# Optimization experiments

Hardware: AMD Instinct MI355X
Metric: run time of the kernel (lower is better)

## Reference

```python
import jax, jax.numpy as jnp
import numpy as np

FEA, DK, H = 768, 64, 12
B, L = 4, 1024
MASK_VAL = -2**15 + 1  # matches torch masked_fill constant


def setup_inputs() -> dict:
    key = jax.random.key(0)
    ks = jax.random.split(key, 16)
    d = {
        'qx': jax.random.normal(ks[0], (B, L, FEA), jnp.float32),
        'kx': jax.random.normal(ks[1], (B, L, FEA), jnp.float32),
        'vx': jax.random.normal(ks[2], (B, L, FEA), jnp.float32),
        'preScores': jax.random.normal(ks[3], (B, H, L, L), jnp.float32),
        'maskPAD': jax.random.randint(ks[4], (B, L, L), 0, 2, jnp.int32),
    }
    s = 1.0 / np.sqrt(FEA)
    d['WQ_w'] = jax.random.normal(ks[5], (H * DK, FEA), jnp.float32) * s
    d['WQ_b'] = jnp.zeros((H * DK,), jnp.float32)
    d['WK_w'] = jax.random.normal(ks[6], (H * DK, FEA), jnp.float32) * s
    d['WK_b'] = jnp.zeros((H * DK,), jnp.float32)
    d['WV_w'] = jax.random.normal(ks[7], (H * DK, FEA), jnp.float32) * s
    d['WV_b'] = jnp.zeros((H * DK,), jnp.float32)
    d['WO_w'] = jax.random.normal(ks[8], (FEA, H * DK), jnp.float32) * s
    d['WO_b'] = jnp.zeros((FEA,), jnp.float32)
    return d


def reference(qx, kx, vx, preScores, maskPAD,
              WQ_w, WQ_b, WK_w, WK_b, WV_w, WV_b, WO_w, WO_b):
    b, l, c = qx.shape
    # projections -> (B, H, L, dk)
    q = (qx @ WQ_w.T + WQ_b).reshape(b, l, H, DK).transpose(0, 2, 1, 3)
    k = (kx @ WK_w.T + WK_b).reshape(b, l, H, DK).transpose(0, 2, 1, 3)
    v = (vx @ WV_w.T + WV_b).reshape(b, l, H, DK).transpose(0, 2, 1, 3)
    scores = jnp.einsum('bhqd,bhkd->bhqk', q, k) / np.sqrt(DK)
    scores = scores + preScores  # RealFormer residual scores
    scores = jnp.where((maskPAD == 0)[:, None, :, :], jnp.float32(MASK_VAL), scores)
    alpha = jax.nn.softmax(scores, axis=3)  # dropout p=0 (eval/deterministic)
    z = jnp.einsum('bhqk,bhkd->bhqd', alpha, v)
    z = z.transpose(0, 2, 1, 3).reshape(b, l, H * DK)
    z = z @ WO_w.T + WO_b
    return z, scores
```

## Files before the change

### kernel.cpp

```cpp
#include <hip/hip_runtime.h>
#include <hip/hip_bf16.h>

#define B_ 4
#define L_ 1024
#define H_ 12
#define DK_ 64
#define FEA_ 768
#define MASKV (-32767.0f)

typedef __attribute__((ext_vector_type(8))) short bf16x8;
typedef __attribute__((ext_vector_type(4))) short s16x4;
typedef __attribute__((ext_vector_type(4))) float f32x4;
typedef unsigned int u32;

__device__ inline short f2bf(float x) {
  __hip_bfloat16 h = __float2bfloat16(x);
  return __builtin_bit_cast(short, h);
}

#define SZX  (4 * 1024 * 768)
#define SZW  (768 * 768)

__global__ __launch_bounds__(256) void k_cvt(
    const float* __restrict__ qx, const float* __restrict__ kx,
    const float* __restrict__ vx,
    const float* __restrict__ Wq, const float* __restrict__ Wk,
    const float* __restrict__ Wv,
    unsigned short* __restrict__ dst)
{
  const size_t SZX4 = SZX / 4, SZW4 = SZW / 4;
  const size_t total4 = 3 * SZX4 + 3 * SZW4;
  for (size_t i4 = (size_t)blockIdx.x * 256 + threadIdx.x; i4 < total4;
       i4 += (size_t)gridDim.x * 256) {
    const float* src; size_t o4; size_t db;
    if (i4 < SZX4)               { src = qx; o4 = i4;               db = 0; }
    else if (i4 < 2 * SZX4)      { src = kx; o4 = i4 - SZX4;        db = (size_t)SZX; }
    else if (i4 < 3 * SZX4)      { src = vx; o4 = i4 - 2 * SZX4;    db = 2 * (size_t)SZX; }
    else if (i4 < 3 * SZX4 + SZW4)     { src = Wq; o4 = i4 - 3 * SZX4;            db = 3 * (size_t)SZX; }
    else if (i4 < 3 * SZX4 + 2 * SZW4) { src = Wk; o4 = i4 - 3 * SZX4 - SZW4;     db = 3 * (size_t)SZX + SZW; }
    else                               { src = Wv; o4 = i4 - 3 * SZX4 - 2 * SZW4; db = 3 * (size_t)SZX + 2 * (size_t)SZW; }
    float4 v = ((const float4*)src)[o4];
    s16x4 r = {f2bf(v.x), f2bf(v.y), f2bf(v.z), f2bf(v.w)};
    *(s16x4*)(dst + db + o4 * 4) = r;
  }
}

__global__ __launch_bounds__(256) void k_proj(
    const unsigned short* __restrict__ qxb, const unsigned short* __restrict__ kxb,
    const unsigned short* __restrict__ vxb,
    const unsigned short* __restrict__ Wqb, const unsigned short* __restrict__ Wkb,
    const unsigned short* __restrict__ Wvb,
    const float* __restrict__ bq, const float* __restrict__ bk,
    const float* __restrict__ bv,
    unsigned short* __restrict__ Qb, unsigned short* __restrict__ Kb,
    unsigned short* __restrict__ Vt)
{
  __shared__ short lA[2][64 * 64];
  __shared__ short lB[2][64 * 64];

  const int which = blockIdx.z;
  const unsigned short* __restrict__ Ab = (which == 0) ? qxb : (which == 1) ? kxb : vxb;
  const unsigned short* __restrict__ Wb = (which == 0) ? Wqb : (which == 1) ? Wkb : Wvb;
  const float* __restrict__ bias = (which == 0) ? bq : (which == 1) ? bk : bv;

  const int tid = threadIdx.x;
  const int lane = tid & 63;
  const int wid = tid >> 6;
  const int wr = wid >> 1, wc = wid & 1;
  const int m0 = blockIdx.x * 64;
  const int n0 = blockIdx.y * 64;
  const int g = lane >> 4, qc = lane & 15;
  const int srow = lane >> 3;
  const int spos = lane & 7;

#define PSTAGE(buf, ktof)                                                      \
  {                                                                            \
    _Pragma("unroll")                                                          \
    for (int i_ = 0; i_ < 2; i_++) {                                           \
      int r0_ = wid * 16 + i_ * 8;                                             \
      int row_ = r0_ + srow;                                                   \
      int cs_ = spos ^ (row_ & 7);                                             \
      __builtin_amdgcn_global_load_lds(                                        \
          (const __attribute__((address_space(1))) u32*)(Ab +                  \
              (size_t)(m0 + row_) * FEA_ + (ktof) + cs_ * 8),                  \
          (__attribute__((address_space(3))) u32*)&lA[buf][r0_ * 64],          \
          16, 0, 0);                                                           \
      __builtin_amdgcn_global_load_lds(                                        \
          (const __attribute__((address_space(1))) u32*)(Wb +                  \
              (size_t)(n0 + row_) * FEA_ + (ktof) + cs_ * 8),                  \
          (__attribute__((address_space(3))) u32*)&lB[buf][r0_ * 64],          \
          16, 0, 0);                                                           \
    }                                                                          \
  }

  f32x4 acc[2][2];
#pragma unroll
  for (int i = 0; i < 2; i++)
#pragma unroll
    for (int j = 0; j < 2; j++) acc[i][j] = f32x4{0.f, 0.f, 0.f, 0.f};

  PSTAGE(0, 0);
  asm volatile("s_waitcnt vmcnt(0)" ::: "memory");
  __builtin_amdgcn_s_barrier();

  for (int kt = 0; kt < 12; kt++) {
    const int cur = kt & 1, nxt = cur ^ 1;
    if (kt < 11) PSTAGE(nxt, (kt + 1) * 64);
    __builtin_amdgcn_sched_barrier(0);
    __builtin_amdgcn_s_setprio(1);
#pragma unroll
    for (int s = 0; s < 2; s++) {
      bf16x8 af[2], bfr[2];
#pragma unroll
      for (int i = 0; i < 2; i++) {
        int ar = wr * 32 + i * 16 + qc;
        af[i] = *(const bf16x8*)&lA[cur][ar * 64 + (((s * 4 + g) ^ (ar & 7)) << 3)];
        int br = wc * 32 + i * 16 + qc;
        bfr[i] = *(const bf16x8*)&lB[cur][br * 64 + (((s * 4 + g) ^ (br & 7)) << 3)];
      }
#pragma unroll
      for (int i = 0; i < 2; i++)
#pragma unroll
        for (int j = 0; j < 2; j++)
          acc[i][j] = __builtin_amdgcn_mfma_f32_16x16x32_bf16(af[i], bfr[j], acc[i][j], 0, 0, 0);
    }
    __builtin_amdgcn_s_setprio(0);
    asm volatile("s_waitcnt vmcnt(0)" ::: "memory");
    __builtin_amdgcn_s_barrier();
  }

  const int cn0 = n0 + wc * 32;
  float bv2[2];
#pragma unroll
  for (int j = 0; j < 2; j++) bv2[j] = bias[cn0 + j * 16 + qc];

#pragma unroll
  for (int i = 0; i < 2; i++) {
    int m = m0 + wr * 32 + i * 16 + g * 4;
    int bb = m >> 10;
    int l = m & 1023;
#pragma unroll
    for (int j = 0; j < 2; j++) {
      int n = cn0 + j * 16 + qc;
      int hh = n >> 6, d = n & 63;
#pragma unroll
      for (int r = 0; r < 4; r++) {
        unsigned short v = (unsigned short)f2bf(acc[i][j][r] + bv2[j]);
        if (which == 2) {
          Vt[(((size_t)bb * H_ + hh) * DK_ + d) * L_ + (l + r)] = v;
        } else if (which == 0) {
          Qb[(((size_t)bb * H_ + hh) * L_ + (l + r)) * DK_ + d] = v;
        } else {
          Kb[(((size_t)bb * H_ + hh) * L_ + (l + r)) * DK_ + d] = v;
        }
      }
    }
  }
#undef PSTAGE
}

__global__ __launch_bounds__(256, 3) void k_attn(
    const unsigned short* __restrict__ Qb, const unsigned short* __restrict__ Kb,
    const unsigned short* __restrict__ Vt,
    const float* __restrict__ preScores, const int* __restrict__ maskPAD,
    float* __restrict__ scoresOut, unsigned short* __restrict__ zp)
{
  __shared__ short lK[2][64 * 64];
  __shared__ short lV[2][64 * 64];
  __shared__ short lP[4][16 * 64];

  const int tid = threadIdx.x, lane = tid & 63, wid = tid >> 6;
  const int bi = blockIdx.x;
  const int slot = bi >> 3;
  const int bh_i = (bi & 7) * 6 + (slot >> 4);
  const int qt = slot & 15;
  const int b = bh_i / H_;
  const int h = bh_i % H_;
  const int q0 = qt * 64;
  const int g = lane >> 4, qr = lane & 15;
  const int qrow = q0 + wid * 16 + qr;

  const size_t bh = (size_t)b * H_ + h;
  const unsigned short* __restrict__ Kbh = Kb + bh * L_ * DK_;
  const unsigned short* __restrict__ Vbh = Vt + bh * DK_ * L_;

  const int srow = lane >> 3;
  const int spos = lane & 7;

#define STAGE_KV(buf, kv0)                                                     \
  {                                                                            \
    _Pragma("unroll")                                                          \
    for (int i_ = 0; i_ < 2; i_++) {                                           \
      int r0_ = wid * 16 + i_ * 8;                                             \
      int row_ = r0_ + srow;                                                   \
      int cs_ = spos ^ (row_ & 7);                                             \
      __builtin_amdgcn_global_load_lds(                                        \
          (const __attribute__((address_space(1))) u32*)(Kbh +                 \
              (size_t)((kv0) + row_) * DK_ + cs_ * 8),                         \
          (__attribute__((address_space(3))) u32*)&lK[buf][r0_ * 64],          \
          16, 0, 0);                                                           \
      __builtin_amdgcn_global_load_lds(                                        \
          (const __attribute__((address_space(1))) u32*)(Vbh +                 \
              (size_t)row_ * L_ + (kv0) + cs_ * 8),                            \
          (__attribute__((address_space(3))) u32*)&lV[buf][r0_ * 64],          \
          16, 0, 0);                                                           \
    }                                                                          \
  }

  bf16x8 qf[2];
#pragma unroll
  for (int s = 0; s < 2; s++)
    qf[s] = *(const bf16x8*)(Qb + (bh * L_ + qrow) * DK_ + s * 32 + g * 8);

  f32x4 o[4];
#pragma unroll
  for (int i = 0; i < 4; i++) o[i] = f32x4{0.f, 0.f, 0.f, 0.f};
  float psum = 0.f;

  const size_t psBase = (bh * L_ + qrow) * L_;
  const size_t mkBase = ((size_t)b * L_ + qrow) * L_;

  STAGE_KV(0, 0);
  __builtin_amdgcn_sched_barrier(0);
  float4 psn[4];
  int4 mkn[4];
#pragma unroll
  for (int i = 0; i < 4; i++) {
    psn[i] = *(const float4*)(preScores + psBase + i * 16 + g * 4);
    mkn[i] = *(const int4*)(maskPAD + mkBase + i * 16 + g * 4);
  }
  asm volatile("s_waitcnt vmcnt(8)" ::: "memory");
  __builtin_amdgcn_s_barrier();

  for (int kt = 0; kt < 16; kt++) {
    const int kv0 = kt * 64;
    const int cur = kt & 1, nxt = cur ^ 1;

    if (kt < 15) {
      STAGE_KV(nxt, kv0 + 64);
    }
    __builtin_amdgcn_sched_barrier(0);

    float4 psc[4]; int4 mkc[4];
#pragma unroll
    for (int i = 0; i < 4; i++) { psc[i] = psn[i]; mkc[i] = mkn[i]; }
    if (kt < 15) {
#pragma unroll
      for (int i = 0; i < 4; i++) {
        psn[i] = *(const float4*)(preScores + psBase + kv0 + 64 + i * 16 + g * 4);
        mkn[i] = *(const int4*)(maskPAD + mkBase + kv0 + 64 + i * 16 + g * 4);
      }
    }

    f32x4 st[4];
#pragma unroll
    for (int i = 0; i < 4; i++) st[i] = f32x4{0.f, 0.f, 0.f, 0.f};
    __builtin_amdgcn_s_setprio(1);
#pragma unroll
    for (int s = 0; s < 2; s++) {
#pragma unroll
      for (int i = 0; i < 4; i++) {
        int kr = i * 16 + qr;
        bf16x8 kf = *(const bf16x8*)&lK[cur][kr * 64 + (((s * 4 + g) ^ (kr & 7)) << 3)];
        st[i] = __builtin_amdgcn_mfma_f32_16x16x32_bf16(kf, qf[s], st[i], 0, 0, 0);
      }
    }
    __builtin_amdgcn_s_setprio(0);

#pragma unroll
    for (int i = 0; i < 4; i++) {
      int ko = i * 16 + g * 4;
      float4 sv;
      sv.x = (mkc[i].x == 0) ? MASKV : st[i][0] * 0.125f + psc[i].x;
      sv.y = (mkc[i].y == 0) ? MASKV : st[i][1] * 0.125f + psc[i].y;
      sv.z = (mkc[i].z == 0) ? MASKV : st[i][2] * 0.125f + psc[i].z;
      sv.w = (mkc[i].w == 0) ? MASKV : st[i][3] * 0.125f + psc[i].w;
      *(float4*)(scoresOut + psBase + kv0 + ko) = sv;
      float p0 = __expf(sv.x);
      float p1 = __expf(sv.y);
      float p2 = __expf(sv.z);
      float p3 = __expf(sv.w);
      psum += (p0 + p1) + (p2 + p3);
      s16x4 pw = {f2bf(p0), f2bf(p1), f2bf(p2), f2bf(p3)};
      int c = i * 2 + (g >> 1);
      *(s16x4*)&lP[wid][qr * 64 + ((c ^ (qr & 7)) << 3) + ((g & 1) << 2)] = pw;
    }

    __builtin_amdgcn_s_setprio(1);
#pragma unroll
    for (int s = 0; s < 2; s++) {
      bf16x8 pf = *(const bf16x8*)&lP[wid][qr * 64 + (((s * 4 + g) ^ (qr & 7)) << 3)];
#pragma unroll
      for (int i = 0; i < 4; i++) {
        int vr = i * 16 + qr;
        bf16x8 vf = *(const bf16x8*)&lV[cur][vr * 64 + (((s * 4 + g) ^ (vr & 7)) << 3)];
        o[i] = __builtin_amdgcn_mfma_f32_16x16x32_bf16(vf, pf, o[i], 0, 0, 0);
      }
    }
    __builtin_amdgcn_s_setprio(0);

    asm volatile("s_waitcnt vmcnt(12)" ::: "memory");
    __builtin_amdgcn_s_barrier();
  }

  psum += __shfl_xor(psum, 16);
  psum += __shfl_xor(psum, 32);
  float inv = 1.f / psum;
  size_t zr = ((size_t)b * L_ + qrow) * FEA_ + (size_t)h * DK_;
#pragma unroll
  for (int i = 0; i < 4; i++) {
    s16x4 zw = {f2bf(o[i][0] * inv), f2bf(o[i][1] * inv),
                f2bf(o[i][2] * inv), f2bf(o[i][3] * inv)};
    *(s16x4*)((unsigned short*)zp + zr + i * 16 + g * 4) = zw;
  }
#undef STAGE_KV
}

__global__ __launch_bounds__(256) void k_oproj(
    const unsigned short* __restrict__ zp,
    const float* __restrict__ Wo, const float* __restrict__ bo,
    float* __restrict__ out)
{
  __shared__ short lA[2][64 * 64];
  __shared__ short lB[2][64 * 64];

  const int tid = threadIdx.x;
  const int lane = tid & 63;
  const int wid = tid >> 6;
  const int wr = wid >> 1, wc = wid & 1;
  const int m0 = blockIdx.x * 64;
  const int n0 = blockIdx.y * 64;
  const int g = lane >> 4, qc = lane & 15;
  const int row_s = tid >> 2;
  const int cg = tid & 3;

  bf16x8 rA[2];
  float4 rB[4];

#define OP_LOAD(ktof)                                                          \
  {                                                                            \
    const bf16x8* pa_ = (const bf16x8*)(zp + (size_t)(m0 + row_s) * FEA_ + (ktof) + cg * 16); \
    rA[0] = pa_[0]; rA[1] = pa_[1];                                            \
    const float4* pb_ = (const float4*)(Wo + (size_t)(n0 + row_s) * FEA_ + (ktof) + cg * 16); \
    rB[0] = pb_[0]; rB[1] = pb_[1]; rB[2] = pb_[2]; rB[3] = pb_[3];            \
  }

#define OP_WRITE(buf)                                                          \
  {                                                                            \
    int c0_ = cg * 2, c1_ = cg * 2 + 1;                                        \
    *(bf16x8*)&lA[buf][row_s * 64 + ((c0_ ^ (row_s & 7)) << 3)] = rA[0];       \
    *(bf16x8*)&lA[buf][row_s * 64 + ((c1_ ^ (row_s & 7)) << 3)] = rA[1];       \
    bf16x8 b0_, b1_;                                                           \
    b0_[0] = f2bf(rB[0].x); b0_[1] = f2bf(rB[0].y); b0_[2] = f2bf(rB[0].z); b0_[3] = f2bf(rB[0].w); \
    b0_[4] = f2bf(rB[1].x); b0_[5] = f2bf(rB[1].y); b0_[6] = f2bf(rB[1].z); b0_[7] = f2bf(rB[1].w); \
    b1_[0] = f2bf(rB[2].x); b1_[1] = f2bf(rB[2].y); b1_[2] = f2bf(rB[2].z); b1_[3] = f2bf(rB[2].w); \
    b1_[4] = f2bf(rB[3].x); b1_[5] = f2bf(rB[3].y); b1_[6] = f2bf(rB[3].z); b1_[7] = f2bf(rB[3].w); \
    *(bf16x8*)&lB[buf][row_s * 64 + ((c0_ ^ (row_s & 7)) << 3)] = b0_;         \
    *(bf16x8*)&lB[buf][row_s * 64 + ((c1_ ^ (row_s & 7)) << 3)] = b1_;         \
  }

  f32x4 acc[2][2];
#pragma unroll
  for (int i = 0; i < 2; i++)
#pragma unroll
    for (int j = 0; j < 2; j++) acc[i][j] = f32x4{0.f, 0.f, 0.f, 0.f};

  OP_LOAD(0);
  OP_WRITE(0);
  __syncthreads();

  for (int kt = 0; kt < 12; kt++) {
    const int cur = kt & 1, nxt = cur ^ 1;
    if (kt < 11) OP_LOAD((kt + 1) * 64);
#pragma unroll
    for (int s = 0; s < 2; s++) {
      bf16x8 af[2], bfr[2];
#pragma unroll
      for (int i = 0; i < 2; i++) {
        int ar = wr * 32 + i * 16 + qc;
        af[i] = *(const bf16x8*)&lA[cur][ar * 64 + (((s * 4 + g) ^ (ar & 7)) << 3)];
        int br = wc * 32 + i * 16 + qc;
        bfr[i] = *(const bf16x8*)&lB[cur][br * 64 + (((s * 4 + g) ^ (br & 7)) << 3)];
      }
#pragma unroll
      for (int i = 0; i < 2; i++)
#pragma unroll
        for (int j = 0; j < 2; j++)
          acc[i][j] = __builtin_amdgcn_mfma_f32_16x16x32_bf16(af[i], bfr[j], acc[i][j], 0, 0, 0);
    }
    if (kt < 11) OP_WRITE(nxt);
    __syncthreads();
  }

  const int cn0 = n0 + wc * 32;
  float bv2[2];
#pragma unroll
  for (int j = 0; j < 2; j++) bv2[j] = bo[cn0 + j * 16 + qc];

#pragma unroll
  for (int i = 0; i < 2; i++) {
    int m = m0 + wr * 32 + i * 16 + g * 4;
#pragma unroll
    for (int j = 0; j < 2; j++) {
      int n = cn0 + j * 16 + qc;
#pragma unroll
      for (int r = 0; r < 4; r++) {
        out[(size_t)(m + r) * FEA_ + n] = acc[i][j][r] + bv2[j];
      }
    }
  }
#undef OP_LOAD
#undef OP_WRITE
}

extern "C" void kernel_launch(void* const* d_in, const int* in_sizes, int n_in,
                              void* d_out, int out_size, void* d_ws, size_t ws_size,
                              hipStream_t stream) {
  const float* qx = (const float*)d_in[0];
  const float* kx = (const float*)d_in[1];
  const float* vx = (const float*)d_in[2];
  const float* preScores = (const float*)d_in[3];
  const int* maskPAD = (const int*)d_in[4];
  const float* Wq = (const float*)d_in[5];
  const float* bq = (const float*)d_in[6];
  const float* Wk = (const float*)d_in[7];
  const float* bk = (const float*)d_in[8];
  const float* Wv = (const float*)d_in[9];
  const float* bv = (const float*)d_in[10];
  const float* Wo = (const float*)d_in[11];
  const float* bo = (const float*)d_in[12];

  float* z_out = (float*)d_out;
  float* scores_out = z_out + (size_t)B_ * L_ * FEA_;

  unsigned short* Qb = (unsigned short*)d_ws;
  unsigned short* Kb = Qb + (size_t)B_ * H_ * L_ * DK_;
  unsigned short* Vt = Kb + (size_t)B_ * H_ * L_ * DK_;
  unsigned short* zp = Vt + (size_t)B_ * H_ * L_ * DK_;

  unsigned short* cvtb = (unsigned short*)(scores_out + (50331648 - 5603328));
  const unsigned short* qxb = cvtb;
  const unsigned short* kxb = cvtb + (size_t)SZX;
  const unsigned short* vxb = cvtb + 2 * (size_t)SZX;
  const unsigned short* Wqb = cvtb + 3 * (size_t)SZX;
  const unsigned short* Wkb = cvtb + 3 * (size_t)SZX + (size_t)SZW;
  const unsigned short* Wvb = cvtb + 3 * (size_t)SZX + 2 * (size_t)SZW;

  k_cvt<<<dim3(1024), 256, 0, stream>>>(qx, kx, vx, Wq, Wk, Wv, cvtb);
  k_proj<<<dim3(64, 12, 3), 256, 0, stream>>>(qxb, kxb, vxb, Wqb, Wkb, Wvb,
                                              bq, bk, bv, Qb, Kb, Vt);
  k_attn<<<dim3(8 * 6 * 16, 1, 1), 256, 0, stream>>>(Qb, Kb, Vt, preScores,
                                                     maskPAD, scores_out, zp);
  k_oproj<<<dim3(64, 12), 256, 0, stream>>>(zp, Wo, bo, z_out);
}
```

Before: 181.6 us.

## Pre-convert Wo to bf16 and use direct global-to-LDS loads in output projection

Adds a small kernel that converts the output weight matrix to bf16 into the now-unused Q workspace. The output projection then stages both operands with global_load_lds straight into swizzled shared memory instead of going through registers, and raises wave priority around the MFMA block. The V-transpose store in the projection kernel is also vectorised to 4-element writes. The aim is to cut register traffic and fp32 weight bandwidth in the output GEMM, at the cost of one extra kernel launch and reuse of the Q buffer after attention.

```diff
diff --git a/kernel.cpp b/kernel.cpp
--- a/kernel.cpp
+++ b/kernel.cpp
@@ -45,6 +45,17 @@
   }
 }
 
+__global__ __launch_bounds__(256) void k_cvt2(
+    const float* __restrict__ Wo, unsigned short* __restrict__ dst)
+{
+  size_t i4 = (size_t)blockIdx.x * 256 + threadIdx.x;
+  if (i4 < (size_t)SZW / 4) {
+    float4 v = ((const float4*)Wo)[i4];
+    s16x4 r = {f2bf(v.x), f2bf(v.y), f2bf(v.z), f2bf(v.w)};
+    *(s16x4*)(dst + i4 * 4) = r;
+  }
+}
+
 __global__ __launch_bounds__(256) void k_proj(
     const unsigned short* __restrict__ qxb, const unsigned short* __restrict__ kxb,
     const unsigned short* __restrict__ vxb,
@@ -143,15 +154,19 @@
     for (int j = 0; j < 2; j++) {
       int n = cn0 + j * 16 + qc;
       int hh = n >> 6, d = n & 63;
-#pragma unroll
-      for (int r = 0; r < 4; r++) {
-        unsigned short v = (unsigned short)f2bf(acc[i][j][r] + bv2[j]);
-        if (which == 2) {
-          Vt[(((size_t)bb * H_ + hh) * DK_ + d) * L_ + (l + r)] = v;
-        } else if (which == 0) {
-          Qb[(((size_t)bb * H_ + hh) * L_ + (l + r)) * DK_ + d] = v;
-        } else {
-          Kb[(((size_t)bb * H_ + hh) * L_ + (l + r)) * DK_ + d] = v;
+      if (which == 2) {
+        s16x4 vv = {f2bf(acc[i][j][0] + bv2[j]), f2bf(acc[i][j][1] + bv2[j]),
+                    f2bf(acc[i][j][2] + bv2[j]), f2bf(acc[i][j][3] + bv2[j])};
+        *(s16x4*)&Vt[(((size_t)bb * H_ + hh) * DK_ + d) * L_ + l] = vv;
+      } else {
+#pragma unroll
+        for (int r = 0; r < 4; r++) {
+          unsigned short v = (unsigned short)f2bf(acc[i][j][r] + bv2[j]);
+          if (which == 0) {
+            Qb[(((size_t)bb * H_ + hh) * L_ + (l + r)) * DK_ + d] = v;
+          } else {
+            Kb[(((size_t)bb * H_ + hh) * L_ + (l + r)) * DK_ + d] = v;
+          }
         }
       }
     }
@@ -318,7 +333,7 @@
 
 __global__ __launch_bounds__(256) void k_oproj(
     const unsigned short* __restrict__ zp,
-    const float* __restrict__ Wo, const float* __restrict__ bo,
+    const unsigned short* __restrict__ Wob, const float* __restrict__ bo,
     float* __restrict__ out)
 {
   __shared__ short lA[2][64 * 64];
@@ -331,32 +346,27 @@
   const int m0 = blockIdx.x * 64;
   const int n0 = blockIdx.y * 64;
   const int g = lane >> 4, qc = lane & 15;
-  const int row_s = tid >> 2;
-  const int cg = tid & 3;
-
-  bf16x8 rA[2];
-  float4 rB[4];
-
-#define OP_LOAD(ktof)                                                          \
+  const int srow = lane >> 3;
+  const int spos = lane & 7;
+
+#define OSTAGE(buf, ktof)                                                      \
   {                                                                            \
-    const bf16x8* pa_ = (const bf16x8*)(zp + (size_t)(m0 + row_s) * FEA_ + (ktof) + cg * 16); \
-    rA[0] = pa_[0]; rA[1] = pa_[1];                                            \
-    const float4* pb_ = (const float4*)(Wo + (size_t)(n0 + row_s) * FEA_ + (ktof) + cg * 16); \
-    rB[0] = pb_[0]; rB[1] = pb_[1]; rB[2] = pb_[2]; rB[3] = pb_[3];            \
-  }
-
-#define OP_WRITE(buf)                                                          \
-  {                                                                            \
-    int c0_ = cg * 2, c1_ = cg * 2 + 1;                                        \
-    *(bf16x8*)&lA[buf][row_s * 64 + ((c0_ ^ (row_s & 7)) << 3)] = rA[0];       \
-    *(bf16x8*)&lA[buf][row_s * 64 + ((c1_ ^ (row_s & 7)) << 3)] = rA[1];       \
-    bf16x8 b0_, b1_;                                                           \
-    b0_[0] = f2bf(rB[0].x); b0_[1] = f2bf(rB[0].y); b0_[2] = f2bf(rB[0].z); b0_[3] = f2bf(rB[0].w); \
-    b0_[4] = f2bf(rB[1].x); b0_[5] = f2bf(rB[1].y); b0_[6] = f2bf(rB[1].z); b0_[7] = f2bf(rB[1].w); \
-    b1_[0] = f2bf(rB[2].x); b1_[1] = f2bf(rB[2].y); b1_[2] = f2bf(rB[2].z); b1_[3] = f2bf(rB[2].w); \
-    b1_[4] = f2bf(rB[3].x); b1_[5] = f2bf(rB[3].y); b1_[6] = f2bf(rB[3].z); b1_[7] = f2bf(rB[3].w); \
-    *(bf16x8*)&lB[buf][row_s * 64 + ((c0_ ^ (row_s & 7)) << 3)] = b0_;         \
-    *(bf16x8*)&lB[buf][row_s * 64 + ((c1_ ^ (row_s & 7)) << 3)] = b1_;         \
+    _Pragma("unroll")                                                          \
+    for (int i_ = 0; i_ < 2; i_++) {                                           \
+      int r0_ = wid * 16 + i_ * 8;                                             \
+      int row_ = r0_ + srow;                                                   \
+      int cs_ = spos ^ (row_ & 7);                                             \
+      __builtin_amdgcn_global_load_lds(                                        \
+          (const __attribute__((address_space(1))) u32*)(zp +                  \
+              (size_t)(m0 + row_) * FEA_ + (ktof) + cs_ * 8),                  \
+          (__attribute__((address_space(3))) u32*)&lA[buf][r0_ * 64],          \
+          16, 0, 0);                                                           \
+      __builtin_amdgcn_global_load_lds(                                        \
+          (const __attribute__((address_space(1))) u32*)(Wob +                 \
+              (size_t)(n0 + row_) * FEA_ + (ktof) + cs_ * 8),                  \
+          (__attribute__((address_space(3))) u32*)&lB[buf][r0_ * 64],          \
+          16, 0, 0);                                                           \
+    }                                                                          \
   }
 
   f32x4 acc[2][2];
@@ -365,13 +375,15 @@
 #pragma unroll
     for (int j = 0; j < 2; j++) acc[i][j] = f32x4{0.f, 0.f, 0.f, 0.f};
 
-  OP_LOAD(0);
-  OP_WRITE(0);
-  __syncthreads();
+  OSTAGE(0, 0);
+  asm volatile("s_waitcnt vmcnt(0)" ::: "memory");
+  __builtin_amdgcn_s_barrier();
 
   for (int kt = 0; kt < 12; kt++) {
     const int cur = kt & 1, nxt = cur ^ 1;
-    if (kt < 11) OP_LOAD((kt + 1) * 64);
+    if (kt < 11) OSTAGE(nxt, (kt + 1) * 64);
+    __builtin_amdgcn_sched_barrier(0);
+    __builtin_amdgcn_s_setprio(1);
 #pragma unroll
     for (int s = 0; s < 2; s++) {
       bf16x8 af[2], bfr[2];
@@ -388,8 +400,9 @@
         for (int j = 0; j < 2; j++)
           acc[i][j] = __builtin_amdgcn_mfma_f32_16x16x32_bf16(af[i], bfr[j], acc[i][j], 0, 0, 0);
     }
-    if (kt < 11) OP_WRITE(nxt);
-    __syncthreads();
+    __builtin_amdgcn_s_setprio(0);
+    asm volatile("s_waitcnt vmcnt(0)" ::: "memory");
+    __builtin_amdgcn_s_barrier();
   }
 
   const int cn0 = n0 + wc * 32;
@@ -409,8 +422,7 @@
       }
     }
   }
-#undef OP_LOAD
-#undef OP_WRITE
+#undef OSTAGE
 }
 
 extern "C" void kernel_launch(void* const* d_in, const int* in_sizes, int n_in,
@@ -446,10 +458,13 @@
   const unsigned short* Wkb = cvtb + 3 * (size_t)SZX + (size_t)SZW;
   const unsigned short* Wvb = cvtb + 3 * (size_t)SZX + 2 * (size_t)SZW;
 
+  unsigned short* Wob = Qb;
+
   k_cvt<<<dim3(1024), 256, 0, stream>>>(qx, kx, vx, Wq, Wk, Wv, cvtb);
   k_proj<<<dim3(64, 12, 3), 256, 0, stream>>>(qxb, kxb, vxb, Wqb, Wkb, Wvb,
                                               bq, bk, bv, Qb, Kb, Vt);
   k_attn<<<dim3(8 * 6 * 16, 1, 1), 256, 0, stream>>>(Qb, Kb, Vt, preScores,
                                                      maskPAD, scores_out, zp);
-  k_oproj<<<dim3(64, 12), 256, 0, stream>>>(zp, Wo, bo, z_out);
-}
+  k_cvt2<<<dim3(576), 256, 0, stream>>>(Wo, Wob);
+  k_oproj<<<dim3(64, 12), 256, 0, stream>>>(zp, Wob, bo, z_out);
+}
```

Result: faster. 169.2 us (-6.8%).
